# Kernel optimization log

Measured on AMD Instinct MI355X. Metric: run time of the kernel, lower is better.

The kernel has to match this reference:

```python
import jax, jax.numpy as jnp
import numpy as np

N_BASIS = 8
CUTOFF = 5.0
NORM_FACTOR = 16.0


def setup_inputs() -> dict:
    key = jax.random.key(0)
    ks = jax.random.split(key, 10)
    N, E, C = 20000, 320000, 32
    s = 1.0 / np.sqrt(C)
    return {
        "node0": jax.random.normal(ks[0], (N, C), jnp.float32),
        "node1": jax.random.normal(ks[1], (N, C, 3), jnp.float32),
        "node2": jax.random.normal(ks[2], (N, C, 3, 3), jnp.float32),
        "rij": jax.random.normal(ks[3], (E, 3), jnp.float32) * 1.5,
        "Wrad": jax.random.normal(ks[4], (11, N_BASIS, C), jnp.float32) * 0.3,
        "U": jax.random.normal(ks[5], (3, C, C), jnp.float32) * s,
        "V": jax.random.normal(ks[6], (8, C, C), jnp.float32) * s,
        "Wg": jax.random.normal(ks[7], (3, C, C), jnp.float32) * s,
        "idx_i": jax.random.randint(ks[8], (E,), 0, N),
        "idx_j": jax.random.randint(ks[9], (E,), 0, N),
    }


def reference(node0, node1, node2, rij, Wrad, U, V, Wg, idx_i, idx_j):
    N, C = node0.shape
    # radial basis (Gaussian RBF * cosine cutoff envelope)
    dist = jnp.sqrt(jnp.sum(rij * rij, -1) + 1e-12)           # [E]
    rhat = rij / dist[:, None]                                 # [E,3]
    centers = jnp.linspace(0.5, CUTOFF, N_BASIS, dtype=node0.dtype)
    fc = 0.5 * (jnp.cos(jnp.pi * jnp.clip(dist / CUTOFF, 0.0, 1.0)) + 1.0)
    rbf = jnp.exp(-4.0 * (dist[:, None] - centers) ** 2) * fc[:, None]  # [E,B]
    # per-coupling-path radial filters: 11 paths (in_way, r_way, out_way)
    w = jnp.einsum('eb,pbc->pec', rbf, Wrad)                   # [11,E,C]
    # gather neighbor (node_j) features per edge
    g0 = node0[idx_j]                                          # [E,C]
    g1 = node1[idx_j]                                          # [E,C,3]
    g2 = node2[idx_j]                                          # [E,C,3,3]
    m1 = rhat                                                  # [E,3]
    m2 = rhat[:, :, None] * rhat[:, None, :]                   # [E,3,3]
    # graph conv: contract node_j tensor with r-way moment, weighted by radial filter
    # paths: 0:(0,0,0) 1:(0,1,1) 2:(0,2,2) 3:(1,0,1) 4:(1,1,0) 5:(1,1,2)
    #        6:(1,2,1) 7:(2,0,2) 8:(2,1,1) 9:(2,2,0) 10:(2,2,2)
    msg0 = (g0 * w[0]
            + jnp.einsum('eca,ea->ec', g1, m1) * w[4]
            + jnp.einsum('ecab,eab->ec', g2, m2) * w[9])
    msg1 = (jnp.einsum('ec,ea->eca', g0 * w[1], m1)
            + g1 * w[3][:, :, None]
            + jnp.einsum('eca,eab->ecb', g1, m2) * w[6][:, :, None]
            + jnp.einsum('ecab,eb->eca', g2, m1) * w[8][:, :, None])
    msg2 = (jnp.einsum('ec,eab->ecab', g0 * w[2], m2)
            + jnp.einsum('eca,eb->ecab', g1 * w[5][:, :, None], m1)
            + g2 * w[7][:, :, None, None]
            + jnp.einsum('ecab,ebd->ecad', g2, m2) * w[10][:, :, None, None])
    # scatter_add aggregation into per-atom features, normalized
    a0 = jax.ops.segment_sum(msg0, idx_i, num_segments=N) / NORM_FACTOR
    a1 = jax.ops.segment_sum(msg1, idx_i, num_segments=N) / NORM_FACTOR
    a2 = jax.ops.segment_sum(msg2, idx_i, num_segments=N) / NORM_FACTOR
    # multi-body self-interaction (2-body linear U + 3-body products V)
    y0 = (jnp.einsum('nc,cd->nd', a0, U[0])
          + jnp.einsum('nc,cd->nd', a0 * a0, V[0])
          + jnp.einsum('nc,cd->nd', jnp.einsum('nca,nca->nc', a1, a1), V[3])
          + jnp.einsum('nc,cd->nd', jnp.einsum('ncab,ncab->nc', a2, a2), V[6]))
    y1 = (jnp.einsum('nca,cd->nda', a1, U[1])
          + jnp.einsum('nca,cd->nda', a0[:, :, None] * a1, V[1])
          + jnp.einsum('nca,cd->nda', jnp.einsum('nca,ncab->ncb', a1, a2), V[5]))
    y2 = (jnp.einsum('ncab,cd->ndab', a2, U[2])
          + jnp.einsum('ncab,cd->ndab', a0[:, :, None, None] * a2, V[2])
          + jnp.einsum('ncab,cd->ndab', a1[:, :, :, None] * a1[:, :, None, :], V[4])
          + jnp.einsum('ncab,cd->ndab', jnp.einsum('ncab,ncbd->ncad', a2, a2), V[7]))
    # gated nonlinearity (scalar channel gates tensor ways) + residual add
    new0 = node0 + jax.nn.silu(y0 @ Wg[0])
    new1 = node1 + y1 * jax.nn.silu(y0 @ Wg[1])[:, :, None]
    new2 = node2 + y2 * jax.nn.silu(y0 @ Wg[2])[:, :, None, None]
    return (new0, new1, new2)
```

## Files before the change

### kernel.cpp

```cpp
#include <hip/hip_runtime.h>
#include <hip/hip_fp16.h>

#define NCH 32
#define NB 8
#define NPB 8

typedef __attribute__((ext_vector_type(2))) _Float16 half2r;

__device__ __forceinline__ unsigned short f2h(float f) {
    return __half_as_ushort(__float2half_rn(f));
}
__device__ __forceinline__ float h2f_lo(unsigned int u) {
    half2r v = __builtin_bit_cast(half2r, u);
    return (float)v.x;
}
__device__ __forceinline__ float h2f_hi(unsigned int u) {
    half2r v = __builtin_bit_cast(half2r, u);
    return (float)v.y;
}
__device__ __forceinline__ unsigned int pack2h(float lo, float hi) {
    return (unsigned int)f2h(lo) | ((unsigned int)f2h(hi) << 16);
}

__device__ __forceinline__ float fdot2u(unsigned int a, unsigned int b, float c) {
#if __has_builtin(__builtin_amdgcn_fdot2)
    return __builtin_amdgcn_fdot2(__builtin_bit_cast(half2r, a),
                                  __builtin_bit_cast(half2r, b), c, false);
#else
    half2r av = __builtin_bit_cast(half2r, a);
    half2r bv = __builtin_bit_cast(half2r, b);
    return c + (float)av.x * (float)bv.x + (float)av.y * (float)bv.y;
#endif
}

__device__ __forceinline__ void acc8h(float& y, uint4 w, uint4 f) {
    y = fdot2u(w.x, f.x, y);
    y = fdot2u(w.y, f.y, y);
    y = fdot2u(w.z, f.z, y);
    y = fdot2u(w.w, f.w, y);
}
__device__ __forceinline__ void acc8fh(float& y, uint4 w, float4 a, float4 b) {
    y += h2f_lo(w.x) * a.x + h2f_hi(w.x) * a.y + h2f_lo(w.y) * a.z + h2f_hi(w.y) * a.w
       + h2f_lo(w.z) * b.x + h2f_hi(w.z) * b.y + h2f_lo(w.w) * b.z + h2f_hi(w.w) * b.w;
}

__global__ __launch_bounds__(256) void prep_kernel(
    const float* __restrict__ node0, const float* __restrict__ node1,
    const float* __restrict__ node2,
    const float* __restrict__ U, const float* __restrict__ V,
    const float* __restrict__ Wg, const float* __restrict__ Wrad,
    const int* __restrict__ idx_i, int* __restrict__ cursor,
    uint2* __restrict__ t0g, uint4* __restrict__ t1g,
    unsigned short* __restrict__ t2g,
    unsigned short* __restrict__ wswz, unsigned int* __restrict__ wradp,
    int N, int E, int TB)
{
    __shared__ float s1[8 * 96];
    __shared__ float s2[8 * 288];
    const int bx = blockIdx.x;

    if (bx < TB) {
        const int nb0 = bx * 8;
        const int remN = N - nb0;
        if (remN >= 8) {
            const float4* src1 = reinterpret_cast<const float4*>(node1 + (size_t)nb0 * 96);
            float4* d1 = reinterpret_cast<float4*>(s1);
            for (int i = threadIdx.x; i < 192; i += 256) d1[i] = src1[i];
            const float4* src2 = reinterpret_cast<const float4*>(node2 + (size_t)nb0 * 288);
            float4* d2 = reinterpret_cast<float4*>(s2);
            for (int i = threadIdx.x; i < 576; i += 256) d2[i] = src2[i];
        } else {
            const int tot1 = remN * 96;
            for (int i = threadIdx.x; i < 768; i += 256)
                s1[i] = (i < tot1) ? node1[(size_t)nb0 * 96 + i] : 0.f;
            const int tot2 = remN * 288;
            for (int i = threadIdx.x; i < 2304; i += 256)
                s2[i] = (i < tot2) ? node2[(size_t)nb0 * 288 + i] : 0.f;
        }
        __syncthreads();

        const int g = threadIdx.x >> 5;
        const int c = threadIdx.x & 31;
        const int n = nb0 + g;
        if (n >= N) return;

        float G0 = node0[(size_t)n * 32 + c];
        float G1[3];
        #pragma unroll
        for (int a = 0; a < 3; ++a) G1[a] = s1[g * 96 + c * 3 + a];
        float G2[9];
        #pragma unroll
        for (int k = 0; k < 9; ++k) G2[k] = s2[g * 288 + c * 9 + k];

        const size_t b = ((size_t)n << 5) + c;
        uint2 P0;
        P0.x = pack2h(G0, G1[0]);
        P0.y = pack2h(G1[1], G1[2]);
        uint4 P1;
        P1.x = pack2h(G2[0], G2[1]);
        P1.y = pack2h(G2[2], G2[3]);
        P1.z = pack2h(G2[4], G2[5]);
        P1.w = pack2h(G2[6], G2[7]);
        t0g[b] = P0;
        t1g[b] = P1;
        t2g[b] = f2h(G2[8]);
        return;
    }

    const int r = bx - TB;
    if (r < 56) {
        int idx = r * 256 + threadIdx.x;
        if (idx >= 14 * 1024) return;
        int m = idx >> 10, rr = idx & 1023;
        int c = rr >> 5, d = rr & 31;
        float v;
        if (m < 3)       v = U[m * 1024 + c * 32 + d];
        else if (m < 11) v = V[(m - 3) * 1024 + c * 32 + d];
        else             v = Wg[(m - 11) * 1024 + c * 32 + d];
        wswz[m * 1024 + (c >> 3) * 256 + d * 8 + (c & 7)] = f2h(v);
        return;
    }
    if (r < 62) {
        int idx = (r - 56) * 256 + threadIdx.x;
        if (idx >= 11 * 4 * 32) return;
        int c = idx & 31, bb = (idx >> 5) & 3, p = idx >> 7;
        float lo = Wrad[p * 256 + (2 * bb) * 32 + c] * (1.0f / 16.0f);
        float hi = Wrad[p * 256 + (2 * bb + 1) * 32 + c] * (1.0f / 16.0f);
        wradp[c * 44 + p * 4 + bb] = pack2h(lo, hi);
        return;
    }
    {
        int e = (r - 62) * 256 + threadIdx.x;
        if (e < E) atomicAdd(&cursor[idx_i[e]], 1);
    }
}

__global__ __launch_bounds__(256) void scan_reduce_kernel(
    const int* __restrict__ counts, int* __restrict__ blocksums, int N)
{
    const int tid = threadIdx.x;
    const int base = blockIdx.x * 1024;
    int v = 0;
    #pragma unroll
    for (int k = 0; k < 4; ++k) {
        int i = base + tid * 4 + k;
        if (i < N) v += counts[i];
    }
    #pragma unroll
    for (int off = 1; off < 64; off <<= 1) v += __shfl_xor(v, off, 64);
    __shared__ int wsum[4];
    if ((tid & 63) == 0) wsum[tid >> 6] = v;
    __syncthreads();
    if (tid == 0) blocksums[blockIdx.x] = wsum[0] + wsum[1] + wsum[2] + wsum[3];
}

__global__ void scan_top_kernel(
    const int* __restrict__ blocksums, int* __restrict__ bases,
    int* __restrict__ offsets, int nb, int N)
{
    int l = threadIdx.x;
    int v = (l < nb) ? blocksums[l] : 0;
    int incl = v;
    #pragma unroll
    for (int off = 1; off < 64; off <<= 1) {
        int t = __shfl_up(incl, off, 64);
        if (l >= off) incl += t;
    }
    if (l < nb) bases[l] = incl - v;
    if (l == nb - 1) offsets[N] = incl;
}

__global__ __launch_bounds__(256) void scan_write_kernel(
    int* __restrict__ cursor, const int* __restrict__ bases,
    int* __restrict__ offsets, int N)
{
    const int tid = threadIdx.x;
    const int i0 = blockIdx.x * 1024 + tid * 4;
    int v[4]; int lsum = 0;
    #pragma unroll
    for (int k = 0; k < 4; ++k) {
        int i = i0 + k;
        v[k] = (i < N) ? cursor[i] : 0;
        lsum += v[k];
    }
    int incl = lsum;
    #pragma unroll
    for (int off = 1; off < 64; off <<= 1) {
        int t = __shfl_up(incl, off, 64);
        if ((tid & 63) >= off) incl += t;
    }
    __shared__ int wsum[4];
    if ((tid & 63) == 63) wsum[tid >> 6] = incl;
    __syncthreads();
    int add = bases[blockIdx.x];
    for (int w = 0; w < (tid >> 6); ++w) add += wsum[w];
    int run = add + incl - lsum;
    #pragma unroll
    for (int k = 0; k < 4; ++k) {
        int i = i0 + k;
        if (i < N) { offsets[i] = run; cursor[i] = run; run += v[k]; }
    }
}

__global__ __launch_bounds__(256) void scatter_meta_kernel(
    const int* __restrict__ idx_i, const int* __restrict__ idx_j,
    const float* __restrict__ rij, int* __restrict__ cursor,
    uint2* __restrict__ mh, uint4* __restrict__ mr, int E)
{
    int e = blockIdx.x * 256 + threadIdx.x;
    if (e >= E) return;
    float rx = rij[3 * e + 0], ry = rij[3 * e + 1], rz = rij[3 * e + 2];
    float sq = rx * rx + ry * ry + rz * rz + 1e-12f;
    float inv = rsqrtf(sq);
    float dist = sq * inv;
    float tcl = fminf(dist * 0.2f, 1.0f);
    float fc = 0.5f * (__cosf(3.14159265358979f * tcl) + 1.0f);
    float rbf[NB];
    #pragma unroll
    for (int b = 0; b < NB; ++b) {
        float dd = dist - (0.5f + (float)b * (4.5f / 7.0f));
        rbf[b] = __expf(-4.0f * dd * dd) * fc;
    }
    const int i = idx_i[e];
    const unsigned int j = (unsigned int)idx_j[e];
    int slot = atomicAdd(&cursor[i], 1);
    mh[slot] = make_uint2(pack2h(rx * inv, ry * inv),
                          (unsigned int)f2h(rz * inv) | (j << 16));
    mr[slot] = make_uint4(pack2h(rbf[0], rbf[1]), pack2h(rbf[2], rbf[3]),
                          pack2h(rbf[4], rbf[5]), pack2h(rbf[6], rbf[7]));
}

__device__ __forceinline__ void edge_compute(
    uint2 P0, uint4 P1, unsigned short g28, uint2 H, uint4 R,
    const uint4 wrq[11], float& A0, float (&A1)[3], float (&A2)[9])
{
    const float h0 = h2f_lo(H.x), h1 = h2f_hi(H.x), h2 = h2f_lo(H.y);

    float w[11];
    #pragma unroll
    for (int p = 0; p < 11; ++p)
        w[p] = fdot2u(R.x, wrq[p].x,
               fdot2u(R.y, wrq[p].y,
               fdot2u(R.z, wrq[p].z,
               fdot2u(R.w, wrq[p].w, 0.0f))));

    const float G0 = h2f_lo(P0.x);
    float G1[3];
    G1[0] = h2f_hi(P0.x); G1[1] = h2f_lo(P0.y); G1[2] = h2f_hi(P0.y);
    float G2[9];
    G2[0] = h2f_lo(P1.x); G2[1] = h2f_hi(P1.x);
    G2[2] = h2f_lo(P1.y); G2[3] = h2f_hi(P1.y);
    G2[4] = h2f_lo(P1.z); G2[5] = h2f_hi(P1.z);
    G2[6] = h2f_lo(P1.w); G2[7] = h2f_hi(P1.w);
    G2[8] = __half2float(__ushort_as_half(g28));

    const float hh[3] = {h0, h1, h2};
    const float s1 = G1[0] * h0 + G1[1] * h1 + G1[2] * h2;
    float tt[3];
    #pragma unroll
    for (int a = 0; a < 3; ++a)
        tt[a] = G2[a * 3 + 0] * h0 + G2[a * 3 + 1] * h1 + G2[a * 3 + 2] * h2;
    const float s2 = tt[0] * h0 + tt[1] * h1 + tt[2] * h2;

    A0 += G0 * w[0] + s1 * w[4] + s2 * w[9];
    #pragma unroll
    for (int a = 0; a < 3; ++a)
        A1[a] += (G0 * w[1] + s1 * w[6]) * hh[a] + G1[a] * w[3] + tt[a] * w[8];
    #pragma unroll
    for (int a = 0; a < 3; ++a) {
        float pre = G0 * w[2] * hh[a] + G1[a] * w[5] + tt[a] * w[10];
        #pragma unroll
        for (int b = 0; b < 3; ++b)
            A2[a * 3 + b] += pre * hh[b] + G2[a * 3 + b] * w[7];
    }
}

__global__ __launch_bounds__(256) void aggregate_kernel(
    const uint2* __restrict__ t0g, const uint4* __restrict__ t1g,
    const unsigned short* __restrict__ t2g, const unsigned int* __restrict__ wradp,
    const uint2* __restrict__ mh, const uint4* __restrict__ mr,
    const int* __restrict__ offsets,
    float* __restrict__ a0, float* __restrict__ a1, float* __restrict__ a2,
    int N)
{
    const int lane = threadIdx.x & 63;
    const int c = lane & 31;
    const int side = lane >> 5;
    const int n = blockIdx.x * 4 + (threadIdx.x >> 6);
    if (n >= N) return;

    uint4 wrq[11];
    {
        const uint4* wrv = reinterpret_cast<const uint4*>(wradp) + c * 11;
        #pragma unroll
        for (int p = 0; p < 11; ++p) wrq[p] = wrv[p];
    }

    const int beg = offsets[n], end = offsets[n + 1];
    const int deg = end - beg;

    float A0 = 0.f;
    float A1[3] = {0.f, 0.f, 0.f};
    float A2[9] = {0.f, 0.f, 0.f, 0.f, 0.f, 0.f, 0.f, 0.f, 0.f};

    if (deg > 0) {
        const int last = end - 1;
        int eA = beg + side;
        int eB = eA + 2;

        uint2 HA, HB, MHA, MHB;
        uint2 P0A, P0B; uint4 P1A, P1B; unsigned short s2A, s2B;
        uint4 RA, RB;
        {
            const int em = min(eA, last);
            HA = mh[em];
            const size_t b = ((size_t)(HA.y >> 16) << 5) + c;
            P0A = t0g[b]; P1A = t1g[b]; s2A = t2g[b];
            RA = mr[em];
            MHA = mh[min(eA + 4, last)];
        }
        {
            const int em = min(eB, last);
            HB = mh[em];
            const size_t b = ((size_t)(HB.y >> 16) << 5) + c;
            P0B = t0g[b]; P1B = t1g[b]; s2B = t2g[b];
            RB = mr[em];
            MHB = mh[min(eB + 4, last)];
        }

        const int M = (deg + 3) >> 2;

#define SLOT_STEP(P0s, P1s, s2s, Hs, Rs, MHs, eS)                           \
        {                                                                   \
            const uint2 P0 = P0s; const uint4 P1 = P1s;                     \
            const unsigned short g28 = s2s;                                 \
            const uint2 Hc = Hs; const uint4 Rc = Rs;                       \
            const bool v = (eS < end);                                      \
            const int eSn = eS + 4;                                         \
            {                                                               \
                const size_t b = ((size_t)(MHs.y >> 16) << 5) + c;          \
                P0s = t0g[b]; P1s = t1g[b]; s2s = t2g[b];                   \
                Rs = mr[min(eSn, last)];                                    \
            }                                                               \
            Hs = MHs;                                                       \
            MHs = mh[min(eSn + 4, last)];                                   \
            if (v) edge_compute(P0, P1, g28, Hc, Rc, wrq, A0, A1, A2);      \
            eS = eSn;                                                       \
        }

        for (int m = 0; m < M; ++m) {
            SLOT_STEP(P0A, P1A, s2A, HA, RA, MHA, eA)
            SLOT_STEP(P0B, P1B, s2B, HB, RB, MHB, eB)
        }
#undef SLOT_STEP
    }

    A0 += __shfl_xor(A0, 32, 64);
    #pragma unroll
    for (int a = 0; a < 3; ++a) A1[a] += __shfl_xor(A1[a], 32, 64);
    #pragma unroll
    for (int k = 0; k < 9; ++k) A2[k] += __shfl_xor(A2[k], 32, 64);

    if (side == 0) {
        a0[n * 32 + c] = A0;
        #pragma unroll
        for (int a = 0; a < 3; ++a) a1[n * 96 + a * 32 + c] = A1[a];
        #pragma unroll
        for (int k = 0; k < 9; ++k) a2[n * 288 + k * 32 + c] = A2[k];
    }
}

__global__ __launch_bounds__(256) void node_kernel(
    const float* __restrict__ node0, const float* __restrict__ node1,
    const float* __restrict__ node2, const unsigned short* __restrict__ wswz,
    float* __restrict__ out0, float* __restrict__ out1, float* __restrict__ out2,
    int N)
{
    __shared__ alignas(16) unsigned short feat[NPB * 49 * 32];
    __shared__ alignas(16) float y0s[NPB][32];

    const uint4* __restrict__ W4 = reinterpret_cast<const uint4*>(wswz);

    const int g = threadIdx.x >> 5;
    const int lane = threadIdx.x & 31;
    const int n = blockIdx.x * NPB + g;
    const bool active = (n < N);

    if (active) {
        const int c = lane;
        float A0 = out0[n * 32 + c];
        float A1[3], A2[9];
        #pragma unroll
        for (int a = 0; a < 3; ++a) A1[a] = out1[n * 96 + a * 32 + c];
        #pragma unroll
        for (int k = 0; k < 9; ++k) A2[k] = out2[n * 288 + k * 32 + c];

        unsigned short* F = &feat[g * 49 * 32];
        F[0 * 32 + c] = f2h(A0);
        F[1 * 32 + c] = f2h(A0 * A0);
        F[2 * 32 + c] = f2h(A1[0] * A1[0] + A1[1] * A1[1] + A1[2] * A1[2]);
        float n2 = 0.f;
        #pragma unroll
        for (int k = 0; k < 9; ++k) n2 += A2[k] * A2[k];
        F[3 * 32 + c] = f2h(n2);
        #pragma unroll
        for (int a = 0; a < 3; ++a) {
            F[(4 + a) * 32 + c] = f2h(A1[a]);
            F[(7 + a) * 32 + c] = f2h(A0 * A1[a]);
        }
        #pragma unroll
        for (int b = 0; b < 3; ++b) {
            float s = A1[0] * A2[0 * 3 + b] + A1[1] * A2[1 * 3 + b] + A1[2] * A2[2 * 3 + b];
            F[(10 + b) * 32 + c] = f2h(s);
        }
        #pragma unroll
        for (int k = 0; k < 9; ++k) {
            F[(13 + k) * 32 + c] = f2h(A2[k]);
            F[(22 + k) * 32 + c] = f2h(A0 * A2[k]);
        }
        #pragma unroll
        for (int a = 0; a < 3; ++a)
            #pragma unroll
            for (int b = 0; b < 3; ++b)
                F[(31 + a * 3 + b) * 32 + c] = f2h(A1[a] * A1[b]);
        #pragma unroll
        for (int a = 0; a < 3; ++a)
            #pragma unroll
            for (int dd = 0; dd < 3; ++dd) {
                float s = A2[a * 3 + 0] * A2[0 * 3 + dd] + A2[a * 3 + 1] * A2[1 * 3 + dd]
                        + A2[a * 3 + 2] * A2[2 * 3 + dd];
                F[(40 + a * 3 + dd) * 32 + c] = f2h(s);
            }
    }
    __syncthreads();

    const int d = lane;
    float y0v = 0.f;
    float y1v[3] = {0.f, 0.f, 0.f};
    float y2v[9] = {0.f, 0.f, 0.f, 0.f, 0.f, 0.f, 0.f, 0.f, 0.f};

    if (active) {
        const uint4* F4 = reinterpret_cast<const uint4*>(&feat[g * 49 * 32]);
        for (int q = 0; q < 4; ++q) {
            const int q32d = q * 32 + d;
            acc8h(y0v, W4[0 * 128 + q32d], F4[0 * 4 + q]);
            acc8h(y0v, W4[3 * 128 + q32d], F4[1 * 4 + q]);
            acc8h(y0v, W4[6 * 128 + q32d], F4[2 * 4 + q]);
            acc8h(y0v, W4[9 * 128 + q32d], F4[3 * 4 + q]);
            uint4 wU1 = W4[1 * 128 + q32d];
            uint4 wV1 = W4[4 * 128 + q32d];
            uint4 wV5 = W4[8 * 128 + q32d];
            #pragma unroll
            for (int a = 0; a < 3; ++a) {
                acc8h(y1v[a], wU1, F4[(4 + a) * 4 + q]);
                acc8h(y1v[a], wV1, F4[(7 + a) * 4 + q]);
                acc8h(y1v[a], wV5, F4[(10 + a) * 4 + q]);
            }
            uint4 wU2 = W4[2 * 128 + q32d];
            uint4 wV2 = W4[5 * 128 + q32d];
            uint4 wV4 = W4[7 * 128 + q32d];
            uint4 wV7 = W4[10 * 128 + q32d];
            #pragma unroll
            for (int k = 0; k < 9; ++k) {
                acc8h(y2v[k], wU2, F4[(13 + k) * 4 + q]);
                acc8h(y2v[k], wV2, F4[(22 + k) * 4 + q]);
                acc8h(y2v[k], wV4, F4[(31 + k) * 4 + q]);
                acc8h(y2v[k], wV7, F4[(40 + k) * 4 + q]);
            }
        }
        y0s[g][d] = y0v;
    }
    __syncthreads();

    if (!active) return;

    float t0 = 0.f, t1 = 0.f, t2 = 0.f;
    {
        const float4* Y4 = reinterpret_cast<const float4*>(y0s[g]);
        #pragma unroll
        for (int q = 0; q < 4; ++q) {
            const int q32d = q * 32 + d;
            float4 ya = Y4[2 * q], yb = Y4[2 * q + 1];
            acc8fh(t0, W4[11 * 128 + q32d], ya, yb);
            acc8fh(t1, W4[12 * 128 + q32d], ya, yb);
            acc8fh(t2, W4[13 * 128 + q32d], ya, yb);
        }
    }
    float s0 = t0 / (1.0f + __expf(-t0));
    float s1 = t1 / (1.0f + __expf(-t1));
    float s2 = t2 / (1.0f + __expf(-t2));

    out0[n * 32 + d] = node0[n * 32 + d] + s0;
    #pragma unroll
    for (int a = 0; a < 3; ++a)
        out1[n * 96 + d * 3 + a] = node1[n * 96 + d * 3 + a] + y1v[a] * s1;
    #pragma unroll
    for (int k = 0; k < 9; ++k)
        out2[n * 288 + d * 9 + k] = node2[n * 288 + d * 9 + k] + y2v[k] * s2;
}

extern "C" void kernel_launch(void* const* d_in, const int* in_sizes, int n_in,
                              void* d_out, int out_size, void* d_ws, size_t ws_size,
                              hipStream_t stream)
{
    const float* node0 = (const float*)d_in[0];
    const float* node1 = (const float*)d_in[1];
    const float* node2 = (const float*)d_in[2];
    const float* rij   = (const float*)d_in[3];
    const float* Wrad  = (const float*)d_in[4];
    const float* U     = (const float*)d_in[5];
    const float* V     = (const float*)d_in[6];
    const float* Wg    = (const float*)d_in[7];
    const int* idx_i   = (const int*)d_in[8];
    const int* idx_j   = (const int*)d_in[9];

    const int N = in_sizes[0] / 32;
    const int E = in_sizes[3] / 3;

    float* out0 = (float*)d_out;
    float* out1 = out0 + (size_t)N * 32;
    float* out2 = out1 + (size_t)N * 96;

    size_t off = 0;
    auto walloc = [&](size_t bytes) -> void* {
        off = (off + 63) & ~(size_t)63;
        void* p = (char*)d_ws + off;
        off += bytes;
        return p;
    };
    int*    cursor    = (int*)   walloc((size_t)N * 4);
    int*    offsets   = (int*)   walloc((size_t)(N + 1) * 4);
    int*    blocksums = (int*)   walloc(64 * 4);
    int*    bases     = (int*)   walloc(64 * 4);
    uint2*  mh        = (uint2*) walloc((size_t)E * sizeof(uint2));
    uint4*  mr        = (uint4*) walloc((size_t)E * sizeof(uint4));
    uint2*  t0g       = (uint2*) walloc((size_t)N * 32 * sizeof(uint2));
    uint4*  t1g       = (uint4*) walloc((size_t)N * 32 * sizeof(uint4));
    unsigned short* t2g = (unsigned short*)walloc((size_t)N * 32 * 2);
    unsigned short* wswz = (unsigned short*)walloc(14 * 1024 * 2);
    unsigned int*  wradp = (unsigned int*)walloc(11 * 4 * 32 * 4);
    (void)ws_size;

    const int nb = (N + 1023) / 1024;
    const int TB = (N + 7) / 8;
    const int HB = (E + 255) / 256;

    hipMemsetAsync(cursor, 0, (size_t)N * sizeof(int), stream);

    prep_kernel<<<dim3(TB + 62 + HB), dim3(256), 0, stream>>>(
        node0, node1, node2, U, V, Wg, Wrad, idx_i, cursor,
        t0g, t1g, t2g, wswz, wradp, N, E, TB);
    scan_reduce_kernel<<<dim3(nb), dim3(256), 0, stream>>>(cursor, blocksums, N);
    scan_top_kernel<<<dim3(1), dim3(64), 0, stream>>>(blocksums, bases, offsets, nb, N);
    scan_write_kernel<<<dim3(nb), dim3(256), 0, stream>>>(cursor, bases, offsets, N);
    scatter_meta_kernel<<<dim3((E + 255) / 256), dim3(256), 0, stream>>>(
        idx_i, idx_j, rij, cursor, mh, mr, E);

    aggregate_kernel<<<dim3((N + 3) / 4), dim3(256), 0, stream>>>(
        t0g, t1g, t2g, wradp, mh, mr, offsets, out0, out1, out2, N);

    node_kernel<<<dim3((N + NPB - 1) / NPB), dim3(256), 0, stream>>>(
        node0, node1, node2, wswz, out0, out1, out2, N);
}
```

Before: 249.1 us.

## Fuse edge aggregation and node self-interaction into a single kernel

Merges the aggregate and node kernels so each wavefront aggregates messages for one node and then computes the self-interaction features, the matmuls and the gating in place. The channel-dot work is split across the two half-waves, and partial sums are combined with cross-lane shuffles. This removes the global round trip of the a0/a1/a2 intermediates and one kernel launch. In exchange it adds block-wide syncs after the irregular-degree aggregation loop, so waves in a block wait on the slowest node, and the shared memory and register footprint of the fused kernel may lower occupancy.

```diff
diff --git a/kernel.cpp b/kernel.cpp
--- a/kernel.cpp
+++ b/kernel.cpp
@@ -3,7 +3,6 @@
 
 #define NCH 32
 #define NB 8
-#define NPB 8
 
 typedef __attribute__((ext_vector_type(2))) _Float16 half2r;
 
@@ -275,19 +274,25 @@
     }
 }
 
-__global__ __launch_bounds__(256) void aggregate_kernel(
+__global__ __launch_bounds__(256) void agg_node_kernel(
     const uint2* __restrict__ t0g, const uint4* __restrict__ t1g,
     const unsigned short* __restrict__ t2g, const unsigned int* __restrict__ wradp,
     const uint2* __restrict__ mh, const uint4* __restrict__ mr,
-    const int* __restrict__ offsets,
-    float* __restrict__ a0, float* __restrict__ a1, float* __restrict__ a2,
+    const int* __restrict__ offsets, const unsigned short* __restrict__ wswz,
+    const float* __restrict__ node0, const float* __restrict__ node1,
+    const float* __restrict__ node2,
+    float* __restrict__ out0, float* __restrict__ out1, float* __restrict__ out2,
     int N)
 {
+    __shared__ alignas(16) unsigned short feat[4 * 49 * 32];
+    __shared__ alignas(16) float y0s[4][32];
+
     const int lane = threadIdx.x & 63;
     const int c = lane & 31;
     const int side = lane >> 5;
-    const int n = blockIdx.x * 4 + (threadIdx.x >> 6);
-    if (n >= N) return;
+    const int wid = threadIdx.x >> 6;
+    const int n = blockIdx.x * 4 + wid;
+    const bool active = (n < N);
 
     uint4 wrq[11];
     {
@@ -296,7 +301,8 @@
         for (int p = 0; p < 11; ++p) wrq[p] = wrv[p];
     }
 
-    const int beg = offsets[n], end = offsets[n + 1];
+    int beg = 0, end = 0;
+    if (active) { beg = offsets[n]; end = offsets[n + 1]; }
     const int deg = end - beg;
 
     float A0 = 0.f;
@@ -361,88 +367,60 @@
     #pragma unroll
     for (int k = 0; k < 9; ++k) A2[k] += __shfl_xor(A2[k], 32, 64);
 
-    if (side == 0) {
-        a0[n * 32 + c] = A0;
-        #pragma unroll
-        for (int a = 0; a < 3; ++a) a1[n * 96 + a * 32 + c] = A1[a];
-        #pragma unroll
-        for (int k = 0; k < 9; ++k) a2[n * 288 + k * 32 + c] = A2[k];
-    }
-}
-
-__global__ __launch_bounds__(256) void node_kernel(
-    const float* __restrict__ node0, const float* __restrict__ node1,
-    const float* __restrict__ node2, const unsigned short* __restrict__ wswz,
-    float* __restrict__ out0, float* __restrict__ out1, float* __restrict__ out2,
-    int N)
-{
-    __shared__ alignas(16) unsigned short feat[NPB * 49 * 32];
-    __shared__ alignas(16) float y0s[NPB][32];
+    unsigned short* F = &feat[wid * 49 * 32];
+    if (active) {
+        if (side == 0) {
+            F[0 * 32 + c] = f2h(A0);
+            F[1 * 32 + c] = f2h(A0 * A0);
+            F[2 * 32 + c] = f2h(A1[0] * A1[0] + A1[1] * A1[1] + A1[2] * A1[2]);
+            float n2 = 0.f;
+            #pragma unroll
+            for (int k = 0; k < 9; ++k) n2 += A2[k] * A2[k];
+            F[3 * 32 + c] = f2h(n2);
+            #pragma unroll
+            for (int a = 0; a < 3; ++a) {
+                F[(4 + a) * 32 + c] = f2h(A1[a]);
+                F[(7 + a) * 32 + c] = f2h(A0 * A1[a]);
+            }
+            #pragma unroll
+            for (int b = 0; b < 3; ++b) {
+                float s = A1[0] * A2[0 * 3 + b] + A1[1] * A2[1 * 3 + b] + A1[2] * A2[2 * 3 + b];
+                F[(10 + b) * 32 + c] = f2h(s);
+            }
+            #pragma unroll
+            for (int k = 0; k < 9; ++k) F[(13 + k) * 32 + c] = f2h(A2[k]);
+            #pragma unroll
+            for (int k = 0; k < 3; ++k) F[(22 + k) * 32 + c] = f2h(A0 * A2[k]);
+        } else {
+            #pragma unroll
+            for (int k = 3; k < 9; ++k) F[(22 + k) * 32 + c] = f2h(A0 * A2[k]);
+            #pragma unroll
+            for (int a = 0; a < 3; ++a)
+                #pragma unroll
+                for (int b = 0; b < 3; ++b)
+                    F[(31 + a * 3 + b) * 32 + c] = f2h(A1[a] * A1[b]);
+            #pragma unroll
+            for (int a = 0; a < 3; ++a)
+                #pragma unroll
+                for (int dd = 0; dd < 3; ++dd) {
+                    float s = A2[a * 3 + 0] * A2[0 * 3 + dd] + A2[a * 3 + 1] * A2[1 * 3 + dd]
+                            + A2[a * 3 + 2] * A2[2 * 3 + dd];
+                    F[(40 + a * 3 + dd) * 32 + c] = f2h(s);
+                }
+        }
+    }
+    __syncthreads();
 
     const uint4* __restrict__ W4 = reinterpret_cast<const uint4*>(wswz);
-
-    const int g = threadIdx.x >> 5;
-    const int lane = threadIdx.x & 31;
-    const int n = blockIdx.x * NPB + g;
-    const bool active = (n < N);
-
-    if (active) {
-        const int c = lane;
-        float A0 = out0[n * 32 + c];
-        float A1[3], A2[9];
-        #pragma unroll
-        for (int a = 0; a < 3; ++a) A1[a] = out1[n * 96 + a * 32 + c];
-        #pragma unroll
-        for (int k = 0; k < 9; ++k) A2[k] = out2[n * 288 + k * 32 + c];
-
-        unsigned short* F = &feat[g * 49 * 32];
-        F[0 * 32 + c] = f2h(A0);
-        F[1 * 32 + c] = f2h(A0 * A0);
-        F[2 * 32 + c] = f2h(A1[0] * A1[0] + A1[1] * A1[1] + A1[2] * A1[2]);
-        float n2 = 0.f;
-        #pragma unroll
-        for (int k = 0; k < 9; ++k) n2 += A2[k] * A2[k];
-        F[3 * 32 + c] = f2h(n2);
-        #pragma unroll
-        for (int a = 0; a < 3; ++a) {
-            F[(4 + a) * 32 + c] = f2h(A1[a]);
-            F[(7 + a) * 32 + c] = f2h(A0 * A1[a]);
-        }
-        #pragma unroll
-        for (int b = 0; b < 3; ++b) {
-            float s = A1[0] * A2[0 * 3 + b] + A1[1] * A2[1 * 3 + b] + A1[2] * A2[2 * 3 + b];
-            F[(10 + b) * 32 + c] = f2h(s);
-        }
-        #pragma unroll
-        for (int k = 0; k < 9; ++k) {
-            F[(13 + k) * 32 + c] = f2h(A2[k]);
-            F[(22 + k) * 32 + c] = f2h(A0 * A2[k]);
-        }
-        #pragma unroll
-        for (int a = 0; a < 3; ++a)
-            #pragma unroll
-            for (int b = 0; b < 3; ++b)
-                F[(31 + a * 3 + b) * 32 + c] = f2h(A1[a] * A1[b]);
-        #pragma unroll
-        for (int a = 0; a < 3; ++a)
-            #pragma unroll
-            for (int dd = 0; dd < 3; ++dd) {
-                float s = A2[a * 3 + 0] * A2[0 * 3 + dd] + A2[a * 3 + 1] * A2[1 * 3 + dd]
-                        + A2[a * 3 + 2] * A2[2 * 3 + dd];
-                F[(40 + a * 3 + dd) * 32 + c] = f2h(s);
-            }
-    }
-    __syncthreads();
-
-    const int d = lane;
     float y0v = 0.f;
     float y1v[3] = {0.f, 0.f, 0.f};
     float y2v[9] = {0.f, 0.f, 0.f, 0.f, 0.f, 0.f, 0.f, 0.f, 0.f};
 
     if (active) {
-        const uint4* F4 = reinterpret_cast<const uint4*>(&feat[g * 49 * 32]);
-        for (int q = 0; q < 4; ++q) {
-            const int q32d = q * 32 + d;
+        const uint4* F4 = reinterpret_cast<const uint4*>(&feat[wid * 49 * 32]);
+        for (int qi = 0; qi < 2; ++qi) {
+            const int q = side * 2 + qi;
+            const int q32d = q * 32 + c;
             acc8h(y0v, W4[0 * 128 + q32d], F4[0 * 4 + q]);
             acc8h(y0v, W4[3 * 128 + q32d], F4[1 * 4 + q]);
             acc8h(y0v, W4[6 * 128 + q32d], F4[2 * 4 + q]);
@@ -468,35 +446,47 @@
                 acc8h(y2v[k], wV7, F4[(40 + k) * 4 + q]);
             }
         }
-        y0s[g][d] = y0v;
-    }
+    }
+    y0v += __shfl_xor(y0v, 32, 64);
+    #pragma unroll
+    for (int a = 0; a < 3; ++a) y1v[a] += __shfl_xor(y1v[a], 32, 64);
+    #pragma unroll
+    for (int k = 0; k < 9; ++k) y2v[k] += __shfl_xor(y2v[k], 32, 64);
+
+    if (active && side == 0) y0s[wid][c] = y0v;
     __syncthreads();
 
-    if (!active) return;
-
     float t0 = 0.f, t1 = 0.f, t2 = 0.f;
-    {
-        const float4* Y4 = reinterpret_cast<const float4*>(y0s[g]);
-        #pragma unroll
-        for (int q = 0; q < 4; ++q) {
-            const int q32d = q * 32 + d;
+    if (active) {
+        const float4* Y4 = reinterpret_cast<const float4*>(y0s[wid]);
+        for (int qi = 0; qi < 2; ++qi) {
+            const int q = side * 2 + qi;
+            const int q32d = q * 32 + c;
             float4 ya = Y4[2 * q], yb = Y4[2 * q + 1];
             acc8fh(t0, W4[11 * 128 + q32d], ya, yb);
             acc8fh(t1, W4[12 * 128 + q32d], ya, yb);
             acc8fh(t2, W4[13 * 128 + q32d], ya, yb);
         }
     }
-    float s0 = t0 / (1.0f + __expf(-t0));
-    float s1 = t1 / (1.0f + __expf(-t1));
-    float s2 = t2 / (1.0f + __expf(-t2));
-
-    out0[n * 32 + d] = node0[n * 32 + d] + s0;
-    #pragma unroll
-    for (int a = 0; a < 3; ++a)
-        out1[n * 96 + d * 3 + a] = node1[n * 96 + d * 3 + a] + y1v[a] * s1;
-    #pragma unroll
-    for (int k = 0; k < 9; ++k)
-        out2[n * 288 + d * 9 + k] = node2[n * 288 + d * 9 + k] + y2v[k] * s2;
+    t0 += __shfl_xor(t0, 32, 64);
+    t1 += __shfl_xor(t1, 32, 64);
+    t2 += __shfl_xor(t2, 32, 64);
+
+    if (active) {
+        if (side == 0) {
+            const float s0 = t0 / (1.0f + __expf(-t0));
+            const float s1g = t1 / (1.0f + __expf(-t1));
+            out0[n * 32 + c] = node0[n * 32 + c] + s0;
+            #pragma unroll
+            for (int a = 0; a < 3; ++a)
+                out1[n * 96 + c * 3 + a] = node1[n * 96 + c * 3 + a] + y1v[a] * s1g;
+        } else {
+            const float s2g = t2 / (1.0f + __expf(-t2));
+            #pragma unroll
+            for (int k = 0; k < 9; ++k)
+                out2[n * 288 + c * 9 + k] = node2[n * 288 + c * 9 + k] + y2v[k] * s2g;
+        }
+    }
 }
 
 extern "C" void kernel_launch(void* const* d_in, const int* in_sizes, int n_in,
@@ -556,9 +546,7 @@
     scatter_meta_kernel<<<dim3((E + 255) / 256), dim3(256), 0, stream>>>(
         idx_i, idx_j, rij, cursor, mh, mr, E);
 
-    aggregate_kernel<<<dim3((N + 3) / 4), dim3(256), 0, stream>>>(
-        t0g, t1g, t2g, wradp, mh, mr, offsets, out0, out1, out2, N);
-
-    node_kernel<<<dim3((N + NPB - 1) / NPB), dim3(256), 0, stream>>>(
-        node0, node1, node2, wswz, out0, out1, out2, N);
-}
+    agg_node_kernel<<<dim3((N + 3) / 4), dim3(256), 0, stream>>>(
+        t0g, t1g, t2g, wradp, mh, mr, offsets, wswz,
+        node0, node1, node2, out0, out1, out2, N);
+}
```

Measured after the change: 261.0 us. 4.8% more time.

## Fold scan top into scan write, drop node barriers, coalesce node output stores

Applied to the files above, without the earlier changes.

Removes the single-wavefront scan_top kernel. Each scan_write block now sums the preceding blocksums itself, and block 0 writes the total, which saves one kernel launch and one dependency step. In node_kernel, each 32-lane node group works only on its own LDS slice, so the block-wide __syncthreads are dropped and out-of-range groups return early. Output stores for out1 and out2 are staged through LDS so lanes write consecutive addresses instead of a stride of 3 or 9. The catch is that correctness now relies on intra-wavefront LDS ordering, and the loop over blocksums adds a small serial sum per block.

```diff
diff --git a/kernel.cpp b/kernel.cpp
--- a/kernel.cpp
+++ b/kernel.cpp
@@ -154,25 +154,9 @@
     if (tid == 0) blocksums[blockIdx.x] = wsum[0] + wsum[1] + wsum[2] + wsum[3];
 }
 
-__global__ void scan_top_kernel(
-    const int* __restrict__ blocksums, int* __restrict__ bases,
+__global__ __launch_bounds__(256) void scan_write_kernel(
+    int* __restrict__ cursor, const int* __restrict__ blocksums,
     int* __restrict__ offsets, int nb, int N)
-{
-    int l = threadIdx.x;
-    int v = (l < nb) ? blocksums[l] : 0;
-    int incl = v;
-    #pragma unroll
-    for (int off = 1; off < 64; off <<= 1) {
-        int t = __shfl_up(incl, off, 64);
-        if (l >= off) incl += t;
-    }
-    if (l < nb) bases[l] = incl - v;
-    if (l == nb - 1) offsets[N] = incl;
-}
-
-__global__ __launch_bounds__(256) void scan_write_kernel(
-    int* __restrict__ cursor, const int* __restrict__ bases,
-    int* __restrict__ offsets, int N)
 {
     const int tid = threadIdx.x;
     const int i0 = blockIdx.x * 1024 + tid * 4;
@@ -192,13 +176,19 @@
     __shared__ int wsum[4];
     if ((tid & 63) == 63) wsum[tid >> 6] = incl;
     __syncthreads();
-    int add = bases[blockIdx.x];
+    int add = 0;
+    for (int b = 0; b < blockIdx.x; ++b) add += blocksums[b];
     for (int w = 0; w < (tid >> 6); ++w) add += wsum[w];
     int run = add + incl - lsum;
     #pragma unroll
     for (int k = 0; k < 4; ++k) {
         int i = i0 + k;
         if (i < N) { offsets[i] = run; cursor[i] = run; run += v[k]; }
+    }
+    if (blockIdx.x == 0 && tid == 0) {
+        int tot = 0;
+        for (int b = 0; b < nb; ++b) tot += blocksums[b];
+        offsets[N] = tot;
     }
 }
 
@@ -376,18 +366,17 @@
     float* __restrict__ out0, float* __restrict__ out1, float* __restrict__ out2,
     int N)
 {
-    __shared__ alignas(16) unsigned short feat[NPB * 49 * 32];
+    __shared__ alignas(16) unsigned short feat[NPB][49 * 32];
     __shared__ alignas(16) float y0s[NPB][32];
 
     const uint4* __restrict__ W4 = reinterpret_cast<const uint4*>(wswz);
 
     const int g = threadIdx.x >> 5;
-    const int lane = threadIdx.x & 31;
+    const int c = threadIdx.x & 31;
     const int n = blockIdx.x * NPB + g;
-    const bool active = (n < N);
-
-    if (active) {
-        const int c = lane;
+    if (n >= N) return;
+
+    {
         float A0 = out0[n * 32 + c];
         float A1[3], A2[9];
         #pragma unroll
@@ -395,7 +384,7 @@
         #pragma unroll
         for (int k = 0; k < 9; ++k) A2[k] = out2[n * 288 + k * 32 + c];
 
-        unsigned short* F = &feat[g * 49 * 32];
+        unsigned short* F = feat[g];
         F[0 * 32 + c] = f2h(A0);
         F[1 * 32 + c] = f2h(A0 * A0);
         F[2 * 32 + c] = f2h(A1[0] * A1[0] + A1[1] * A1[1] + A1[2] * A1[2]);
@@ -432,15 +421,13 @@
                 F[(40 + a * 3 + dd) * 32 + c] = f2h(s);
             }
     }
-    __syncthreads();
-
-    const int d = lane;
+
+    const int d = c;
     float y0v = 0.f;
     float y1v[3] = {0.f, 0.f, 0.f};
     float y2v[9] = {0.f, 0.f, 0.f, 0.f, 0.f, 0.f, 0.f, 0.f, 0.f};
-
-    if (active) {
-        const uint4* F4 = reinterpret_cast<const uint4*>(&feat[g * 49 * 32]);
+    {
+        const uint4* F4 = reinterpret_cast<const uint4*>(feat[g]);
         for (int q = 0; q < 4; ++q) {
             const int q32d = q * 32 + d;
             acc8h(y0v, W4[0 * 128 + q32d], F4[0 * 4 + q]);
@@ -470,9 +457,6 @@
         }
         y0s[g][d] = y0v;
     }
-    __syncthreads();
-
-    if (!active) return;
 
     float t0 = 0.f, t1 = 0.f, t2 = 0.f;
     {
@@ -486,17 +470,32 @@
             acc8fh(t2, W4[13 * 128 + q32d], ya, yb);
         }
     }
-    float s0 = t0 / (1.0f + __expf(-t0));
-    float s1 = t1 / (1.0f + __expf(-t1));
-    float s2 = t2 / (1.0f + __expf(-t2));
+    const float s0 = t0 / (1.0f + __expf(-t0));
+    const float s1g = t1 / (1.0f + __expf(-t1));
+    const float s2g = t2 / (1.0f + __expf(-t2));
 
     out0[n * 32 + d] = node0[n * 32 + d] + s0;
-    #pragma unroll
-    for (int a = 0; a < 3; ++a)
-        out1[n * 96 + d * 3 + a] = node1[n * 96 + d * 3 + a] + y1v[a] * s1;
-    #pragma unroll
-    for (int k = 0; k < 9; ++k)
-        out2[n * 288 + d * 9 + k] = node2[n * 288 + d * 9 + k] + y2v[k] * s2;
+
+    float* yb = reinterpret_cast<float*>(feat[g]);
+    #pragma unroll
+    for (int a = 0; a < 3; ++a) yb[c * 13 + a] = y1v[a] * s1g;
+    #pragma unroll
+    for (int k = 0; k < 9; ++k) yb[c * 13 + 3 + k] = y2v[k] * s2g;
+
+    const size_t b1 = (size_t)n * 96;
+    #pragma unroll
+    for (int it = 0; it < 3; ++it) {
+        const int lin = it * 32 + c;
+        const int ch = lin / 3, a = lin - ch * 3;
+        out1[b1 + lin] = node1[b1 + lin] + yb[ch * 13 + a];
+    }
+    const size_t b2 = (size_t)n * 288;
+    #pragma unroll
+    for (int it = 0; it < 9; ++it) {
+        const int lin = it * 32 + c;
+        const int ch = lin / 9, k = lin - ch * 9;
+        out2[b2 + lin] = node2[b2 + lin] + yb[ch * 13 + 3 + k];
+    }
 }
 
 extern "C" void kernel_launch(void* const* d_in, const int* in_sizes, int n_in,
@@ -531,7 +530,6 @@
     int*    cursor    = (int*)   walloc((size_t)N * 4);
     int*    offsets   = (int*)   walloc((size_t)(N + 1) * 4);
     int*    blocksums = (int*)   walloc(64 * 4);
-    int*    bases     = (int*)   walloc(64 * 4);
     uint2*  mh        = (uint2*) walloc((size_t)E * sizeof(uint2));
     uint4*  mr        = (uint4*) walloc((size_t)E * sizeof(uint4));
     uint2*  t0g       = (uint2*) walloc((size_t)N * 32 * sizeof(uint2));
@@ -551,8 +549,8 @@
         node0, node1, node2, U, V, Wg, Wrad, idx_i, cursor,
         t0g, t1g, t2g, wswz, wradp, N, E, TB);
     scan_reduce_kernel<<<dim3(nb), dim3(256), 0, stream>>>(cursor, blocksums, N);
-    scan_top_kernel<<<dim3(1), dim3(64), 0, stream>>>(blocksums, bases, offsets, nb, N);
-    scan_write_kernel<<<dim3(nb), dim3(256), 0, stream>>>(cursor, bases, offsets, N);
+    scan_write_kernel<<<dim3(nb), dim3(256), 0, stream>>>(
+        cursor, blocksums, offsets, nb, N);
     scatter_meta_kernel<<<dim3((E + 255) / 256), dim3(256), 0, stream>>>(
         idx_i, idx_j, rij, cursor, mh, mr, E);
 
```

New measurement: 250.2 us. About the same (+0.5%).

## Recompute RBF per edge in aggregate from distance; merge scan top into write

Applied to the files above, without the earlier changes.

The scatter step now stores a compact 12-byte edge record (direction in fp16, neighbor index, fp32 distance) in place of separate 8-byte and 16-byte records, so the 8 radial basis values are no longer stored and reloaded. The aggregate kernel rebuilds them per edge from the distance, using one exp for the base Gaussian and a geometric recurrence with precomputed per-basis factors. The scan_top kernel is dropped, and each scan_write block sums the preceding block sums itself. This cuts edge-metadata traffic and one launch, at the cost of extra per-edge ALU work duplicated across lanes and a recurrence formulation with slightly different rounding.

```diff
diff --git a/kernel.cpp b/kernel.cpp
--- a/kernel.cpp
+++ b/kernel.cpp
@@ -6,6 +6,7 @@
 #define NPB 8
 
 typedef __attribute__((ext_vector_type(2))) _Float16 half2r;
+typedef __attribute__((ext_vector_type(2))) __fp16 fp16v2;
 
 __device__ __forceinline__ unsigned short f2h(float f) {
     return __half_as_ushort(__float2half_rn(f));
@@ -20,6 +21,14 @@
 }
 __device__ __forceinline__ unsigned int pack2h(float lo, float hi) {
     return (unsigned int)f2h(lo) | ((unsigned int)f2h(hi) << 16);
+}
+__device__ __forceinline__ unsigned int pkrtz(float lo, float hi) {
+#if __has_builtin(__builtin_amdgcn_cvt_pkrtz)
+    fp16v2 t = __builtin_amdgcn_cvt_pkrtz(lo, hi);
+    return __builtin_bit_cast(unsigned int, t);
+#else
+    return pack2h(lo, hi);
+#endif
 }
 
 __device__ __forceinline__ float fdot2u(unsigned int a, unsigned int b, float c) {
@@ -154,25 +163,9 @@
     if (tid == 0) blocksums[blockIdx.x] = wsum[0] + wsum[1] + wsum[2] + wsum[3];
 }
 
-__global__ void scan_top_kernel(
-    const int* __restrict__ blocksums, int* __restrict__ bases,
+__global__ __launch_bounds__(256) void scan_write_kernel(
+    int* __restrict__ cursor, const int* __restrict__ blocksums,
     int* __restrict__ offsets, int nb, int N)
-{
-    int l = threadIdx.x;
-    int v = (l < nb) ? blocksums[l] : 0;
-    int incl = v;
-    #pragma unroll
-    for (int off = 1; off < 64; off <<= 1) {
-        int t = __shfl_up(incl, off, 64);
-        if (l >= off) incl += t;
-    }
-    if (l < nb) bases[l] = incl - v;
-    if (l == nb - 1) offsets[N] = incl;
-}
-
-__global__ __launch_bounds__(256) void scan_write_kernel(
-    int* __restrict__ cursor, const int* __restrict__ bases,
-    int* __restrict__ offsets, int N)
 {
     const int tid = threadIdx.x;
     const int i0 = blockIdx.x * 1024 + tid * 4;
@@ -192,7 +185,8 @@
     __shared__ int wsum[4];
     if ((tid & 63) == 63) wsum[tid >> 6] = incl;
     __syncthreads();
-    int add = bases[blockIdx.x];
+    int add = 0;
+    for (int b = 0; b < blockIdx.x; ++b) add += blocksums[b];
     for (int w = 0; w < (tid >> 6); ++w) add += wsum[w];
     int run = add + incl - lsum;
     #pragma unroll
@@ -200,12 +194,17 @@
         int i = i0 + k;
         if (i < N) { offsets[i] = run; cursor[i] = run; run += v[k]; }
     }
+    if (blockIdx.x == 0 && tid == 0) {
+        int tot = 0;
+        for (int b = 0; b < nb; ++b) tot += blocksums[b];
+        offsets[N] = tot;
+    }
 }
 
 __global__ __launch_bounds__(256) void scatter_meta_kernel(
     const int* __restrict__ idx_i, const int* __restrict__ idx_j,
     const float* __restrict__ rij, int* __restrict__ cursor,
-    uint2* __restrict__ mh, uint4* __restrict__ mr, int E)
+    uint3* __restrict__ me, int E)
 {
     int e = blockIdx.x * 256 + threadIdx.x;
     if (e >= E) return;
@@ -213,36 +212,44 @@
     float sq = rx * rx + ry * ry + rz * rz + 1e-12f;
     float inv = rsqrtf(sq);
     float dist = sq * inv;
-    float tcl = fminf(dist * 0.2f, 1.0f);
-    float fc = 0.5f * (__cosf(3.14159265358979f * tcl) + 1.0f);
-    float rbf[NB];
-    #pragma unroll
-    for (int b = 0; b < NB; ++b) {
-        float dd = dist - (0.5f + (float)b * (4.5f / 7.0f));
-        rbf[b] = __expf(-4.0f * dd * dd) * fc;
-    }
     const int i = idx_i[e];
     const unsigned int j = (unsigned int)idx_j[e];
     int slot = atomicAdd(&cursor[i], 1);
-    mh[slot] = make_uint2(pack2h(rx * inv, ry * inv),
-                          (unsigned int)f2h(rz * inv) | (j << 16));
-    mr[slot] = make_uint4(pack2h(rbf[0], rbf[1]), pack2h(rbf[2], rbf[3]),
-                          pack2h(rbf[4], rbf[5]), pack2h(rbf[6], rbf[7]));
+    uint3 rec;
+    rec.x = pack2h(rx * inv, ry * inv);
+    rec.y = (unsigned int)f2h(rz * inv) | (j << 16);
+    rec.z = __float_as_uint(dist);
+    me[slot] = rec;
 }
 
 __device__ __forceinline__ void edge_compute(
-    uint2 P0, uint4 P1, unsigned short g28, uint2 H, uint4 R,
-    const uint4 wrq[11], float& A0, float (&A1)[3], float (&A2)[9])
-{
-    const float h0 = h2f_lo(H.x), h1 = h2f_hi(H.x), h2 = h2f_lo(H.y);
+    uint2 P0, uint4 P1, unsigned short g28, uint3 ME,
+    const uint4 wrq[11], const float rbc[7],
+    float& A0, float (&A1)[3], float (&A2)[9])
+{
+    const float h0 = h2f_lo(ME.x), h1 = h2f_hi(ME.x), h2 = h2f_lo(ME.y);
+    const float d  = __uint_as_float(ME.z);
+
+    const float dc = fminf(d, 5.0f);
+    const float fc = 0.5f * (__cosf(0.6283185307f * dc) + 1.0f);
+    const float u  = 2.0f * dc - 1.0f;
+    float f[8];
+    f[0] = fc * __expf(-u * u);
+    const float q = __expf(2.5714285714f * u);
+    #pragma unroll
+    for (int b = 0; b < 7; ++b) f[b + 1] = f[b] * (q * rbc[b]);
+    const unsigned int rb01 = pkrtz(f[0], f[1]);
+    const unsigned int rb23 = pkrtz(f[2], f[3]);
+    const unsigned int rb45 = pkrtz(f[4], f[5]);
+    const unsigned int rb67 = pkrtz(f[6], f[7]);
 
     float w[11];
     #pragma unroll
     for (int p = 0; p < 11; ++p)
-        w[p] = fdot2u(R.x, wrq[p].x,
-               fdot2u(R.y, wrq[p].y,
-               fdot2u(R.z, wrq[p].z,
-               fdot2u(R.w, wrq[p].w, 0.0f))));
+        w[p] = fdot2u(rb01, wrq[p].x,
+               fdot2u(rb23, wrq[p].y,
+               fdot2u(rb45, wrq[p].z,
+               fdot2u(rb67, wrq[p].w, 0.0f))));
 
     const float G0 = h2f_lo(P0.x);
     float G1[3];
@@ -278,8 +285,7 @@
 __global__ __launch_bounds__(256) void aggregate_kernel(
     const uint2* __restrict__ t0g, const uint4* __restrict__ t1g,
     const unsigned short* __restrict__ t2g, const unsigned int* __restrict__ wradp,
-    const uint2* __restrict__ mh, const uint4* __restrict__ mr,
-    const int* __restrict__ offsets,
+    const uint3* __restrict__ me, const int* __restrict__ offsets,
     float* __restrict__ a0, float* __restrict__ a1, float* __restrict__ a2,
     int N)
 {
@@ -295,6 +301,9 @@
         #pragma unroll
         for (int p = 0; p < 11; ++p) wrq[p] = wrv[p];
     }
+    float rbc[7];
+    #pragma unroll
+    for (int b = 0; b < 7; ++b) rbc[b] = __expf(-1.6530612245f * (float)(2 * b + 1));
 
     const int beg = offsets[n], end = offsets[n + 1];
     const int deg = end - beg;
@@ -308,49 +317,43 @@
         int eA = beg + side;
         int eB = eA + 2;
 
-        uint2 HA, HB, MHA, MHB;
+        uint3 MEA, MEB, MAn, MBn;
         uint2 P0A, P0B; uint4 P1A, P1B; unsigned short s2A, s2B;
-        uint4 RA, RB;
         {
-            const int em = min(eA, last);
-            HA = mh[em];
-            const size_t b = ((size_t)(HA.y >> 16) << 5) + c;
+            MEA = me[min(eA, last)];
+            const size_t b = ((size_t)(MEA.y >> 16) << 5) + c;
             P0A = t0g[b]; P1A = t1g[b]; s2A = t2g[b];
-            RA = mr[em];
-            MHA = mh[min(eA + 4, last)];
+            MAn = me[min(eA + 4, last)];
         }
         {
-            const int em = min(eB, last);
-            HB = mh[em];
-            const size_t b = ((size_t)(HB.y >> 16) << 5) + c;
+            MEB = me[min(eB, last)];
+            const size_t b = ((size_t)(MEB.y >> 16) << 5) + c;
             P0B = t0g[b]; P1B = t1g[b]; s2B = t2g[b];
-            RB = mr[em];
-            MHB = mh[min(eB + 4, last)];
+            MBn = me[min(eB + 4, last)];
         }
 
         const int M = (deg + 3) >> 2;
 
-#define SLOT_STEP(P0s, P1s, s2s, Hs, Rs, MHs, eS)                           \
+#define SLOT_STEP(P0s, P1s, s2s, MEs, MNs, eS)                              \
         {                                                                   \
             const uint2 P0 = P0s; const uint4 P1 = P1s;                     \
             const unsigned short g28 = s2s;                                 \
-            const uint2 Hc = Hs; const uint4 Rc = Rs;                       \
+            const uint3 MEc = MEs;                                          \
             const bool v = (eS < end);                                      \
             const int eSn = eS + 4;                                         \
             {                                                               \
-                const size_t b = ((size_t)(MHs.y >> 16) << 5) + c;          \
+                const size_t b = ((size_t)(MNs.y >> 16) << 5) + c;          \
                 P0s = t0g[b]; P1s = t1g[b]; s2s = t2g[b];                   \
-                Rs = mr[min(eSn, last)];                                    \
             }                                                               \
-            Hs = MHs;                                                       \
-            MHs = mh[min(eSn + 4, last)];                                   \
-            if (v) edge_compute(P0, P1, g28, Hc, Rc, wrq, A0, A1, A2);      \
+            MEs = MNs;                                                      \
+            MNs = me[min(eSn + 4, last)];                                   \
+            if (v) edge_compute(P0, P1, g28, MEc, wrq, rbc, A0, A1, A2);    \
             eS = eSn;                                                       \
         }
 
         for (int m = 0; m < M; ++m) {
-            SLOT_STEP(P0A, P1A, s2A, HA, RA, MHA, eA)
-            SLOT_STEP(P0B, P1B, s2B, HB, RB, MHB, eB)
+            SLOT_STEP(P0A, P1A, s2A, MEA, MAn, eA)
+            SLOT_STEP(P0B, P1B, s2B, MEB, MBn, eB)
         }
 #undef SLOT_STEP
     }
@@ -531,9 +534,7 @@
     int*    cursor    = (int*)   walloc((size_t)N * 4);
     int*    offsets   = (int*)   walloc((size_t)(N + 1) * 4);
     int*    blocksums = (int*)   walloc(64 * 4);
-    int*    bases     = (int*)   walloc(64 * 4);
-    uint2*  mh        = (uint2*) walloc((size_t)E * sizeof(uint2));
-    uint4*  mr        = (uint4*) walloc((size_t)E * sizeof(uint4));
+    uint3*  me        = (uint3*) walloc((size_t)E * sizeof(uint3));
     uint2*  t0g       = (uint2*) walloc((size_t)N * 32 * sizeof(uint2));
     uint4*  t1g       = (uint4*) walloc((size_t)N * 32 * sizeof(uint4));
     unsigned short* t2g = (unsigned short*)walloc((size_t)N * 32 * 2);
@@ -551,13 +552,13 @@
         node0, node1, node2, U, V, Wg, Wrad, idx_i, cursor,
         t0g, t1g, t2g, wswz, wradp, N, E, TB);
     scan_reduce_kernel<<<dim3(nb), dim3(256), 0, stream>>>(cursor, blocksums, N);
-    scan_top_kernel<<<dim3(1), dim3(64), 0, stream>>>(blocksums, bases, offsets, nb, N);
-    scan_write_kernel<<<dim3(nb), dim3(256), 0, stream>>>(cursor, bases, offsets, N);
+    scan_write_kernel<<<dim3(nb), dim3(256), 0, stream>>>(
+        cursor, blocksums, offsets, nb, N);
     scatter_meta_kernel<<<dim3((E + 255) / 256), dim3(256), 0, stream>>>(
-        idx_i, idx_j, rij, cursor, mh, mr, E);
+        idx_i, idx_j, rij, cursor, me, E);
 
     aggregate_kernel<<<dim3((N + 3) / 4), dim3(256), 0, stream>>>(
-        t0g, t1g, t2g, wradp, mh, mr, offsets, out0, out1, out2, N);
+        t0g, t1g, t2g, wradp, me, offsets, out0, out1, out2, N);
 
     node_kernel<<<dim3((N + NPB - 1) / NPB), dim3(256), 0, stream>>>(
         node0, node1, node2, wswz, out0, out1, out2, N);
```

Measured after the change: 252.1 us. About the same (+1.2%).
